# Optimization experiments

Measured on AMD Instinct MI355X. Metric: run time of the kernel, lower is better.

Reference implementation:

```python
import jax, jax.numpy as jnp
import numpy as np

MARGIN = 0.2
N_CLASSES = 100
BETA_INIT = 1.2
EPS = 1e-8


def setup_inputs() -> dict:
    key = jax.random.key(0)
    k1, k2, k3 = jax.random.split(key, 3)
    BS, DIM, T = 4096, 128, 500000
    batch = jax.random.normal(k1, (BS, DIM), dtype=jnp.float32)
    labels = jax.random.randint(k2, (BS,), 0, N_CLASSES, dtype=jnp.int64)
    triplets = jax.random.randint(k3, (T, 3), 0, BS, dtype=jnp.int64)
    beta = jnp.ones((N_CLASSES,), dtype=jnp.float32) * BETA_INIT
    return {"batch": batch, "labels": labels, "triplets": triplets, "beta": beta}


def reference(batch, labels, triplets, beta):
    # Gather anchor/positive/negative embedding rows: [T, DIM]
    a = batch[triplets[:, 0]]
    p = batch[triplets[:, 1]]
    n = batch[triplets[:, 2]]
    # Euclidean distances with the module's 1e-8 stabilizer: [T]
    d_ap = jnp.sqrt(jnp.sum((a - p) ** 2, axis=-1) + EPS)
    d_an = jnp.sqrt(jnp.sum((a - n) ** 2, axis=-1) + EPS)
    # Learned per-class beta, indexed by the anchor's label: [T]
    b = beta[labels[triplets[:, 0]]]
    pos_loss = jax.nn.relu(d_ap - b + MARGIN)
    neg_loss = jax.nn.relu(b - d_an + MARGIN)
    pair_count = (jnp.sum((pos_loss > 0.0).astype(jnp.float32))
                  + jnp.sum((neg_loss > 0.0).astype(jnp.float32)))
    total = jnp.sum(pos_loss + neg_loss)
    # If no active pairs, torch code returns the (zero) unnormalized sum.
    return jnp.where(pair_count > 0.0, total / jnp.maximum(pair_count, 1.0), total)
```

## Files before the change

kernel.cpp:

```cpp
#include <hip/hip_runtime.h>

#define MARGIN 0.2f
#define EPS 1e-8f
#define GRID_BLOCKS 2048

typedef float f32x2 __attribute__((ext_vector_type(2)));


__global__ __launch_bounds__(256) void prep_kernel(
    const float* __restrict__ batch,
    const int* __restrict__ labels,
    const int* __restrict__ triplets,
    const float* __restrict__ beta,
    unsigned char* __restrict__ batch8,
    int4* __restrict__ prep,
    int n8, int T)
{
    int i = blockIdx.x * blockDim.x + threadIdx.x;
    if (i < n8) {
        const float4* src = (const float4*)(batch + (size_t)i * 8);
        float4 f0 = src[0];
        float4 f1 = src[1];
        int lo = __builtin_amdgcn_cvt_pk_fp8_f32(f0.x, f0.y, 0, false);
        lo     = __builtin_amdgcn_cvt_pk_fp8_f32(f0.z, f0.w, lo, true);
        int hi = __builtin_amdgcn_cvt_pk_fp8_f32(f1.x, f1.y, 0, false);
        hi     = __builtin_amdgcn_cvt_pk_fp8_f32(f1.z, f1.w, hi, true);
        uint2 w;
        w.x = (unsigned)lo;
        w.y = (unsigned)hi;
        *(uint2*)(batch8 + (size_t)i * 8) = w;
    }
    if (i < T) {
        int a = triplets[3 * i + 0];
        int p = triplets[3 * i + 1];
        int n = triplets[3 * i + 2];
        float b = beta[labels[a]];
        int4 s;
        s.x = a << 7;
        s.y = p << 7;
        s.z = n << 7;
        s.w = __float_as_int(b);
        prep[i] = s;
    }
}

__global__ __launch_bounds__(256) void triplet_main_kernel(
    const unsigned char* __restrict__ batch8,
    const int4* __restrict__ prep,
    float* __restrict__ partial,
    int T)
{
    const int lane = threadIdx.x & 63;
    const int wid  = threadIdx.x >> 6;
    const int sub  = lane >> 3;
    const int fi   = lane & 7;

    float loss = 0.f, cnt = 0.f;
    const int Tm1 = T - 1;

    auto accum = [&](const uint4& A, const uint4& P, const uint4& N,
                     float& sap, float& san) {
        #pragma unroll
        for (int w = 0; w < 4; ++w) {
            unsigned aw = (&A.x)[w];
            unsigned pw = (&P.x)[w];
            unsigned nw = (&N.x)[w];
            f32x2 a0 = __builtin_amdgcn_cvt_pk_f32_fp8(aw, false);
            f32x2 a1 = __builtin_amdgcn_cvt_pk_f32_fp8(aw, true);
            f32x2 p0 = __builtin_amdgcn_cvt_pk_f32_fp8(pw, false);
            f32x2 p1 = __builtin_amdgcn_cvt_pk_f32_fp8(pw, true);
            f32x2 n0 = __builtin_amdgcn_cvt_pk_f32_fp8(nw, false);
            f32x2 n1 = __builtin_amdgcn_cvt_pk_f32_fp8(nw, true);
            float d;
            d = a0[0] - p0[0]; sap = fmaf(d, d, sap);
            d = a0[1] - p0[1]; sap = fmaf(d, d, sap);
            d = a1[0] - p1[0]; sap = fmaf(d, d, sap);
            d = a1[1] - p1[1]; sap = fmaf(d, d, sap);
            d = a0[0] - n0[0]; san = fmaf(d, d, san);
            d = a0[1] - n0[1]; san = fmaf(d, d, san);
            d = a1[0] - n1[0]; san = fmaf(d, d, san);
            d = a1[1] - n1[1]; san = fmaf(d, d, san);
        }
    };

    for (int base = blockIdx.x * 64; base < T; base += gridDim.x * 64) {
        int tA = base + wid * 16 + sub;
        int tB = tA + 8;
        int cA = tA > Tm1 ? Tm1 : tA;
        int cB = tB > Tm1 ? Tm1 : tB;
        int4 sA = prep[cA];
        int4 sB = prep[cB];

        int boff = fi << 4;
        uint4 AA = *(const uint4*)(batch8 + (size_t)(unsigned)sA.x + boff);
        uint4 PA = *(const uint4*)(batch8 + (size_t)(unsigned)sA.y + boff);
        uint4 NA = *(const uint4*)(batch8 + (size_t)(unsigned)sA.z + boff);
        uint4 AB = *(const uint4*)(batch8 + (size_t)(unsigned)sB.x + boff);
        uint4 PB = *(const uint4*)(batch8 + (size_t)(unsigned)sB.y + boff);
        uint4 NB = *(const uint4*)(batch8 + (size_t)(unsigned)sB.z + boff);

        float sapA = 0.f, sanA = 0.f, sapB = 0.f, sanB = 0.f;
        accum(AA, PA, NA, sapA, sanA);
        accum(AB, PB, NB, sapB, sanB);

        #pragma unroll
        for (int off = 4; off >= 1; off >>= 1) {
            sapA += __shfl_xor(sapA, off);
            sanA += __shfl_xor(sanA, off);
            sapB += __shfl_xor(sapB, off);
            sanB += __shfl_xor(sanB, off);
        }

        float bA = __int_as_float(sA.w);
        float bB = __int_as_float(sB.w);
        float mA = (tA < T) ? 1.f : 0.f;
        float mB = (tB < T) ? 1.f : 0.f;

        float dapA = sqrtf(sapA + EPS), danA = sqrtf(sanA + EPS);
        float posA = fmaxf(dapA - bA + MARGIN, 0.f);
        float negA = fmaxf(bA - danA + MARGIN, 0.f);
        loss += mA * (posA + negA);
        cnt  += mA * ((posA > 0.f ? 1.f : 0.f) + (negA > 0.f ? 1.f : 0.f));

        float dapB = sqrtf(sapB + EPS), danB = sqrtf(sanB + EPS);
        float posB = fmaxf(dapB - bB + MARGIN, 0.f);
        float negB = fmaxf(bB - danB + MARGIN, 0.f);
        loss += mB * (posB + negB);
        cnt  += mB * ((posB > 0.f ? 1.f : 0.f) + (negB > 0.f ? 1.f : 0.f));
    }

    #pragma unroll
    for (int off = 32; off >= 1; off >>= 1) {
        loss += __shfl_down(loss, off);
        cnt  += __shfl_down(cnt, off);
    }
    __shared__ float sl[4], sc[4];
    if (lane == 0) { sl[wid] = loss; sc[wid] = cnt; }
    __syncthreads();
    if (threadIdx.x == 0) {
        partial[blockIdx.x * 2 + 0] = sl[0] + sl[1] + sl[2] + sl[3];
        partial[blockIdx.x * 2 + 1] = sc[0] + sc[1] + sc[2] + sc[3];
    }
}


__global__ __launch_bounds__(256) void triplet_loss_f32_kernel(
    const float* __restrict__ batch,
    const int* __restrict__ labels,
    const int* __restrict__ triplets,
    const float* __restrict__ beta,
    float* __restrict__ partial,
    int T)
{
    const int lane = threadIdx.x & 63;
    const int wid  = threadIdx.x >> 6;
    const int sub  = lane >> 3;
    const int fi   = lane & 7;

    float loss = 0.f, cnt = 0.f;

    for (int base = blockIdx.x * 32; base < T; base += gridDim.x * 32) {
        int t = base + wid * 8 + sub;
        if (t < T) {
            int ai = triplets[3 * t + 0];
            int pi = triplets[3 * t + 1];
            int ni = triplets[3 * t + 2];
            float b = beta[labels[ai]];
            const float4* __restrict__ arow = (const float4*)(batch + ((size_t)ai << 7));
            const float4* __restrict__ prow = (const float4*)(batch + ((size_t)pi << 7));
            const float4* __restrict__ nrow = (const float4*)(batch + ((size_t)ni << 7));
            float sap = 0.f, san = 0.f;
            #pragma unroll
            for (int k = 0; k < 4; ++k) {
                float4 av = arow[fi + 8 * k];
                float4 pv = prow[fi + 8 * k];
                float4 nv = nrow[fi + 8 * k];
                float d;
                d = av.x - pv.x; sap += d * d;
                d = av.y - pv.y; sap += d * d;
                d = av.z - pv.z; sap += d * d;
                d = av.w - pv.w; sap += d * d;
                d = av.x - nv.x; san += d * d;
                d = av.y - nv.y; san += d * d;
                d = av.z - nv.z; san += d * d;
                d = av.w - nv.w; san += d * d;
            }
            #pragma unroll
            for (int off = 4; off >= 1; off >>= 1) {
                sap += __shfl_xor(sap, off);
                san += __shfl_xor(san, off);
            }
            float d_ap = sqrtf(sap + EPS);
            float d_an = sqrtf(san + EPS);
            float pos = fmaxf(d_ap - b + MARGIN, 0.f);
            float neg = fmaxf(b - d_an + MARGIN, 0.f);
            loss += pos + neg;
            cnt  += (pos > 0.f ? 1.f : 0.f) + (neg > 0.f ? 1.f : 0.f);
        }
    }

    #pragma unroll
    for (int off = 32; off >= 1; off >>= 1) {
        loss += __shfl_down(loss, off);
        cnt  += __shfl_down(cnt, off);
    }
    __shared__ float sl[4], sc[4];
    if (lane == 0) { sl[wid] = loss; sc[wid] = cnt; }
    __syncthreads();
    if (threadIdx.x == 0) {
        partial[blockIdx.x * 2 + 0] = sl[0] + sl[1] + sl[2] + sl[3];
        partial[blockIdx.x * 2 + 1] = sc[0] + sc[1] + sc[2] + sc[3];
    }
}


__global__ __launch_bounds__(1024) void triplet_finalize_kernel(
    const float* __restrict__ partial, float* __restrict__ out, int nblocks,
    float scale)
{
    float L = 0.f, C = 0.f;
    for (int i = threadIdx.x; i < nblocks; i += blockDim.x) {
        L += partial[2 * i + 0];
        C += partial[2 * i + 1];
    }
    #pragma unroll
    for (int off = 32; off >= 1; off >>= 1) {
        L += __shfl_down(L, off);
        C += __shfl_down(C, off);
    }
    __shared__ float sl[16], sc[16];
    int wid  = threadIdx.x >> 6;
    int lane = threadIdx.x & 63;
    int nw   = blockDim.x >> 6;
    if (lane == 0) { sl[wid] = L; sc[wid] = C; }
    __syncthreads();
    if (threadIdx.x == 0) {
        float Lt = 0.f, Ct = 0.f;
        for (int i = 0; i < nw; ++i) { Lt += sl[i]; Ct += sc[i]; }
        Lt *= scale;
        Ct *= scale;
        out[0] = (Ct > 0.f) ? (Lt / fmaxf(Ct, 1.f)) : Lt;
    }
}

extern "C" void kernel_launch(void* const* d_in, const int* in_sizes, int n_in,
                              void* d_out, int out_size, void* d_ws, size_t ws_size,
                              hipStream_t stream) {
    const float* batch    = (const float*)d_in[0];
    const int*   labels   = (const int*)d_in[1];
    const int*   triplets = (const int*)d_in[2];
    const float* beta     = (const float*)d_in[3];
    float* out = (float*)d_out;

    int nbatch = in_sizes[0];
    int T = in_sizes[2] / 3;

    size_t f8_bytes   = ((size_t)nbatch + 255) & ~(size_t)255;
    size_t prep_bytes = ((size_t)T * sizeof(int4) + 255) & ~(size_t)255;
    size_t need = f8_bytes + prep_bytes + (size_t)GRID_BLOCKS * 2 * sizeof(float);

    if (ws_size >= need) {
        unsigned char* batch8 = (unsigned char*)d_ws;
        int4* prep            = (int4*)((char*)d_ws + f8_bytes);
        float* partial        = (float*)((char*)d_ws + f8_bytes + prep_bytes);

        int n8 = nbatch / 8;
        int prep_items = (T > n8) ? T : n8;
        prep_kernel<<<(prep_items + 255) / 256, 256, 0, stream>>>(
            batch, labels, triplets, beta, batch8, prep, n8, T);

        int grid = GRID_BLOCKS;
        int groups = (T + 63) / 64;
        if (grid > groups) grid = groups;
        triplet_main_kernel<<<grid, 256, 0, stream>>>(batch8, prep, partial, T);
        triplet_finalize_kernel<<<1, 1024, 0, stream>>>(partial, out, grid, 0.125f);
    } else {
        float* partial = (float*)d_ws;
        int grid = GRID_BLOCKS;
        int groups = (T + 31) / 32;
        if (grid > groups) grid = groups;
        triplet_loss_f32_kernel<<<grid, 256, 0, stream>>>(batch, labels, triplets, beta, partial, T);
        triplet_finalize_kernel<<<1, 1024, 0, stream>>>(partial, out, grid, 0.125f);
    }
}
```

Before: 31.67 us.

## Software-pipeline triplet loop with prefetched indices and rows, halve grid

Restructures the main loop so each wave handles one triplet per sub-group per iteration. The prep record is fetched two iterations ahead and the anchor/positive/negative fp8 rows one iteration ahead, so gather latency overlaps the distance math. The grid drops from 2048 to 1024 blocks and each iteration covers 32 triplets per block. In exchange, each iteration does less independent work (one triplet instead of two) and register pressure rises from the carried prefetch buffers.

```diff
diff --git a/kernel.cpp b/kernel.cpp
--- a/kernel.cpp
+++ b/kernel.cpp
@@ -2,7 +2,7 @@
 
 #define MARGIN 0.2f
 #define EPS 1e-8f
-#define GRID_BLOCKS 2048
+#define GRID_BLOCKS 1024
 
 typedef float f32x2 __attribute__((ext_vector_type(2)));
 
@@ -54,10 +54,18 @@
     const int wid  = threadIdx.x >> 6;
     const int sub  = lane >> 3;
     const int fi   = lane & 7;
+    const int boff = fi << 4;
+
+    const int stride = gridDim.x * 32;
+    const int myoff  = wid * 8 + sub;
+    const int Tm1 = T - 1;
 
     float loss = 0.f, cnt = 0.f;
-    const int Tm1 = T - 1;
-
+
+    auto cl = [&](int t) { return t > Tm1 ? Tm1 : t; };
+    auto ldrow = [&](int off) {
+        return *(const uint4*)(batch8 + (size_t)(unsigned)off + boff);
+    };
     auto accum = [&](const uint4& A, const uint4& P, const uint4& N,
                      float& sap, float& san) {
         #pragma unroll
@@ -83,50 +91,40 @@
         }
     };
 
-    for (int base = blockIdx.x * 64; base < T; base += gridDim.x * 64) {
-        int tA = base + wid * 16 + sub;
-        int tB = tA + 8;
-        int cA = tA > Tm1 ? Tm1 : tA;
-        int cB = tB > Tm1 ? Tm1 : tB;
-        int4 sA = prep[cA];
-        int4 sB = prep[cB];
-
-        int boff = fi << 4;
-        uint4 AA = *(const uint4*)(batch8 + (size_t)(unsigned)sA.x + boff);
-        uint4 PA = *(const uint4*)(batch8 + (size_t)(unsigned)sA.y + boff);
-        uint4 NA = *(const uint4*)(batch8 + (size_t)(unsigned)sA.z + boff);
-        uint4 AB = *(const uint4*)(batch8 + (size_t)(unsigned)sB.x + boff);
-        uint4 PB = *(const uint4*)(batch8 + (size_t)(unsigned)sB.y + boff);
-        uint4 NB = *(const uint4*)(batch8 + (size_t)(unsigned)sB.z + boff);
-
-        float sapA = 0.f, sanA = 0.f, sapB = 0.f, sanB = 0.f;
-        accum(AA, PA, NA, sapA, sanA);
-        accum(AB, PB, NB, sapB, sanB);
+    int base = blockIdx.x * 32;
+    int t = base + myoff;
+
+    int4 sc = prep[cl(t)];
+    int4 sn = prep[cl(t + stride)];
+    uint4 Ac = ldrow(sc.x);
+    uint4 Pc = ldrow(sc.y);
+    uint4 Nc = ldrow(sc.z);
+
+    for (; base < T; base += stride, t += stride) {
+        int4 sn2 = prep[cl(t + 2 * stride)];
+        uint4 An = ldrow(sn.x);
+        uint4 Pn = ldrow(sn.y);
+        uint4 Nn = ldrow(sn.z);
+
+        float sap = 0.f, san = 0.f;
+        accum(Ac, Pc, Nc, sap, san);
 
         #pragma unroll
         for (int off = 4; off >= 1; off >>= 1) {
-            sapA += __shfl_xor(sapA, off);
-            sanA += __shfl_xor(sanA, off);
-            sapB += __shfl_xor(sapB, off);
-            sanB += __shfl_xor(sanB, off);
+            sap += __shfl_xor(sap, off);
+            san += __shfl_xor(san, off);
         }
 
-        float bA = __int_as_float(sA.w);
-        float bB = __int_as_float(sB.w);
-        float mA = (tA < T) ? 1.f : 0.f;
-        float mB = (tB < T) ? 1.f : 0.f;
-
-        float dapA = sqrtf(sapA + EPS), danA = sqrtf(sanA + EPS);
-        float posA = fmaxf(dapA - bA + MARGIN, 0.f);
-        float negA = fmaxf(bA - danA + MARGIN, 0.f);
-        loss += mA * (posA + negA);
-        cnt  += mA * ((posA > 0.f ? 1.f : 0.f) + (negA > 0.f ? 1.f : 0.f));
-
-        float dapB = sqrtf(sapB + EPS), danB = sqrtf(sanB + EPS);
-        float posB = fmaxf(dapB - bB + MARGIN, 0.f);
-        float negB = fmaxf(bB - danB + MARGIN, 0.f);
-        loss += mB * (posB + negB);
-        cnt  += mB * ((posB > 0.f ? 1.f : 0.f) + (negB > 0.f ? 1.f : 0.f));
+        float b = __int_as_float(sc.w);
+        float m = (t < T) ? 1.f : 0.f;
+        float dap = sqrtf(sap + EPS), dan = sqrtf(san + EPS);
+        float pos = fmaxf(dap - b + MARGIN, 0.f);
+        float neg = fmaxf(b - dan + MARGIN, 0.f);
+        loss += m * (pos + neg);
+        cnt  += m * ((pos > 0.f ? 1.f : 0.f) + (neg > 0.f ? 1.f : 0.f));
+
+        sc = sn; sn = sn2;
+        Ac = An; Pc = Pn; Nc = Nn;
     }
 
     #pragma unroll
@@ -134,12 +132,12 @@
         loss += __shfl_down(loss, off);
         cnt  += __shfl_down(cnt, off);
     }
-    __shared__ float sl[4], sc[4];
-    if (lane == 0) { sl[wid] = loss; sc[wid] = cnt; }
+    __shared__ float sl[4], sc_[4];
+    if (lane == 0) { sl[wid] = loss; sc_[wid] = cnt; }
     __syncthreads();
     if (threadIdx.x == 0) {
         partial[blockIdx.x * 2 + 0] = sl[0] + sl[1] + sl[2] + sl[3];
-        partial[blockIdx.x * 2 + 1] = sc[0] + sc[1] + sc[2] + sc[3];
+        partial[blockIdx.x * 2 + 1] = sc_[0] + sc_[1] + sc_[2] + sc_[3];
     }
 }
 
@@ -270,7 +268,7 @@
             batch, labels, triplets, beta, batch8, prep, n8, T);
 
         int grid = GRID_BLOCKS;
-        int groups = (T + 63) / 64;
+        int groups = (T + 31) / 32;
         if (grid > groups) grid = groups;
         triplet_main_kernel<<<grid, 256, 0, stream>>>(batch8, prep, partial, T);
         triplet_finalize_kernel<<<1, 1024, 0, stream>>>(partial, out, grid, 0.125f);
```

Result: slower. 33.13 us (+4.6%).

## Fuse triplet index prep into main kernel and finalize via atomic ticket

Applied to the files above, without the earlier changes.

Removes the separate prep pass that wrote a per-triplet int4 record of shifted indices and beta, so the main kernel now reads triplet indices, labels and beta directly. The finalize kernel is also dropped: each block atomically adds its partial sums, and the last block, found through an atomic ticket counter, writes the output. The intent is to cut one full write and read of the prep buffer plus one kernel launch. The cost is that the index→label→beta dependent loads now sit on the main kernel's critical path, and float atomic accumulation makes the summation order nondeterministic.

```diff
diff --git a/kernel.cpp b/kernel.cpp
--- a/kernel.cpp
+++ b/kernel.cpp
@@ -7,16 +7,18 @@
 typedef float f32x2 __attribute__((ext_vector_type(2)));
 
 
-__global__ __launch_bounds__(256) void prep_kernel(
+__global__ __launch_bounds__(256) void convert_kernel(
     const float* __restrict__ batch,
-    const int* __restrict__ labels,
-    const int* __restrict__ triplets,
-    const float* __restrict__ beta,
     unsigned char* __restrict__ batch8,
-    int4* __restrict__ prep,
-    int n8, int T)
+    float* __restrict__ acc,
+    int n8)
 {
     int i = blockIdx.x * blockDim.x + threadIdx.x;
+    if (i == 0) {
+        acc[0] = 0.f;
+        acc[1] = 0.f;
+        ((unsigned*)acc)[2] = 0u;
+    }
     if (i < n8) {
         const float4* src = (const float4*)(batch + (size_t)i * 8);
         float4 f0 = src[0];
@@ -30,34 +32,29 @@
         w.y = (unsigned)hi;
         *(uint2*)(batch8 + (size_t)i * 8) = w;
     }
-    if (i < T) {
-        int a = triplets[3 * i + 0];
-        int p = triplets[3 * i + 1];
-        int n = triplets[3 * i + 2];
-        float b = beta[labels[a]];
-        int4 s;
-        s.x = a << 7;
-        s.y = p << 7;
-        s.z = n << 7;
-        s.w = __float_as_int(b);
-        prep[i] = s;
-    }
 }
 
 __global__ __launch_bounds__(256) void triplet_main_kernel(
     const unsigned char* __restrict__ batch8,
-    const int4* __restrict__ prep,
-    float* __restrict__ partial,
+    const int* __restrict__ labels,
+    const int* __restrict__ triplets,
+    const float* __restrict__ beta,
+    float* __restrict__ acc,
+    float* __restrict__ out,
     int T)
 {
     const int lane = threadIdx.x & 63;
     const int wid  = threadIdx.x >> 6;
     const int sub  = lane >> 3;
     const int fi   = lane & 7;
+    const int boff = fi << 4;
 
     float loss = 0.f, cnt = 0.f;
     const int Tm1 = T - 1;
 
+    auto ldrow = [&](int row) {
+        return *(const uint4*)(batch8 + ((size_t)(unsigned)row << 7) + boff);
+    };
     auto accum = [&](const uint4& A, const uint4& P, const uint4& N,
                      float& sap, float& san) {
         #pragma unroll
@@ -88,16 +85,26 @@
         int tB = tA + 8;
         int cA = tA > Tm1 ? Tm1 : tA;
         int cB = tB > Tm1 ? Tm1 : tB;
-        int4 sA = prep[cA];
-        int4 sB = prep[cB];
-
-        int boff = fi << 4;
-        uint4 AA = *(const uint4*)(batch8 + (size_t)(unsigned)sA.x + boff);
-        uint4 PA = *(const uint4*)(batch8 + (size_t)(unsigned)sA.y + boff);
-        uint4 NA = *(const uint4*)(batch8 + (size_t)(unsigned)sA.z + boff);
-        uint4 AB = *(const uint4*)(batch8 + (size_t)(unsigned)sB.x + boff);
-        uint4 PB = *(const uint4*)(batch8 + (size_t)(unsigned)sB.y + boff);
-        uint4 NB = *(const uint4*)(batch8 + (size_t)(unsigned)sB.z + boff);
+
+        int aA = triplets[3 * cA + 0];
+        int pA = triplets[3 * cA + 1];
+        int nA = triplets[3 * cA + 2];
+        int aB = triplets[3 * cB + 0];
+        int pB = triplets[3 * cB + 1];
+        int nB = triplets[3 * cB + 2];
+
+        int labA = labels[aA];
+        int labB = labels[aB];
+
+        uint4 AA = ldrow(aA);
+        uint4 PA = ldrow(pA);
+        uint4 NA = ldrow(nA);
+        uint4 AB = ldrow(aB);
+        uint4 PB = ldrow(pB);
+        uint4 NB = ldrow(nB);
+
+        float bA = beta[labA];
+        float bB = beta[labB];
 
         float sapA = 0.f, sanA = 0.f, sapB = 0.f, sanB = 0.f;
         accum(AA, PA, NA, sapA, sanA);
@@ -111,8 +118,6 @@
             sanB += __shfl_xor(sanB, off);
         }
 
-        float bA = __int_as_float(sA.w);
-        float bB = __int_as_float(sB.w);
         float mA = (tA < T) ? 1.f : 0.f;
         float mB = (tB < T) ? 1.f : 0.f;
 
@@ -138,8 +143,18 @@
     if (lane == 0) { sl[wid] = loss; sc[wid] = cnt; }
     __syncthreads();
     if (threadIdx.x == 0) {
-        partial[blockIdx.x * 2 + 0] = sl[0] + sl[1] + sl[2] + sl[3];
-        partial[blockIdx.x * 2 + 1] = sc[0] + sc[1] + sc[2] + sc[3];
+        float L = sl[0] + sl[1] + sl[2] + sl[3];
+        float C = sc[0] + sc[1] + sc[2] + sc[3];
+        atomicAdd(&acc[0], L);
+        atomicAdd(&acc[1], C);
+        __threadfence();
+        unsigned ticket = atomicAdd((unsigned*)acc + 2, 1u);
+        if (ticket == gridDim.x - 1) {
+            __threadfence();
+            float Lt = acc[0] * 0.125f;
+            float Ct = acc[1] * 0.125f;
+            out[0] = (Ct > 0.f) ? (Lt / fmaxf(Ct, 1.f)) : Lt;
+        }
     }
 }
 
@@ -213,7 +228,6 @@
     }
 }
 
-
 __global__ __launch_bounds__(1024) void triplet_finalize_kernel(
     const float* __restrict__ partial, float* __restrict__ out, int nblocks,
     float scale)
@@ -255,25 +269,21 @@
     int nbatch = in_sizes[0];
     int T = in_sizes[2] / 3;
 
-    size_t f8_bytes   = ((size_t)nbatch + 255) & ~(size_t)255;
-    size_t prep_bytes = ((size_t)T * sizeof(int4) + 255) & ~(size_t)255;
-    size_t need = f8_bytes + prep_bytes + (size_t)GRID_BLOCKS * 2 * sizeof(float);
+    size_t f8_bytes = ((size_t)nbatch + 255) & ~(size_t)255;
+    size_t need = f8_bytes + 256;
 
     if (ws_size >= need) {
         unsigned char* batch8 = (unsigned char*)d_ws;
-        int4* prep            = (int4*)((char*)d_ws + f8_bytes);
-        float* partial        = (float*)((char*)d_ws + f8_bytes + prep_bytes);
+        float* acc            = (float*)((char*)d_ws + f8_bytes);
 
         int n8 = nbatch / 8;
-        int prep_items = (T > n8) ? T : n8;
-        prep_kernel<<<(prep_items + 255) / 256, 256, 0, stream>>>(
-            batch, labels, triplets, beta, batch8, prep, n8, T);
+        convert_kernel<<<(n8 + 255) / 256, 256, 0, stream>>>(batch, batch8, acc, n8);
 
         int grid = GRID_BLOCKS;
         int groups = (T + 63) / 64;
         if (grid > groups) grid = groups;
-        triplet_main_kernel<<<grid, 256, 0, stream>>>(batch8, prep, partial, T);
-        triplet_finalize_kernel<<<1, 1024, 0, stream>>>(partial, out, grid, 0.125f);
+        triplet_main_kernel<<<grid, 256, 0, stream>>>(
+            batch8, labels, triplets, beta, acc, out, T);
     } else {
         float* partial = (float*)d_ws;
         int grid = GRID_BLOCKS;
```

Result: slower. 94.07 us (+197.1%).
